# Performance work log

Hardware: AMD Instinct MI355X
Metric: run time of the kernel (lower is better)

The kernel has to match this reference:

```python
import jax, jax.numpy as jnp
import numpy as np

N = 10000
E = 160000
NEG_SLOPE = 0.2
BN_EPS = 1e-5


def _gat_conv(x, W, a_src, a_dst, b, src, dst, n, heads):
    # PyG GATConv, concat=False (mean over heads), shared lin for src/dst.
    H = heads
    C = W.shape[1] // H
    h = (x @ W).reshape(n, H, C)                       # (N,H,C)
    e_s = jnp.einsum('nhc,hc->nh', h, a_src)           # (N,H)
    e_d = jnp.einsum('nhc,hc->nh', h, a_dst)
    alpha = jax.nn.leaky_relu(e_s[src] + e_d[dst], NEG_SLOPE)   # (E',H)
    amax = jax.ops.segment_max(alpha, dst, num_segments=n)       # per-dst softmax
    ex = jnp.exp(alpha - amax[dst])
    denom = jax.ops.segment_sum(ex, dst, num_segments=n)
    w = ex / (denom[dst] + 1e-16)
    out = jax.ops.segment_sum(h[src] * w[:, :, None], dst, num_segments=n)  # (N,H,C)
    return out.mean(axis=1) + b


def _bn(x, g, b):
    mu = x.mean(axis=0)
    var = x.var(axis=0)  # biased, as torch BN training forward
    return (x - mu) * jax.lax.rsqrt(var + BN_EPS) * g + b


def setup_inputs() -> dict:
    key = jax.random.key(0)
    ks = jax.random.split(key, 32)
    d = {}
    d['x'] = jax.random.normal(ks[0], (N, 64), jnp.float32)
    d['edge_index'] = jax.random.randint(ks[1], (2, E), 0, N, jnp.int64)
    s = lambda k, shape, fan: jax.random.normal(k, shape, jnp.float32) * (1.0 / np.sqrt(fan))
    d['Wp'] = s(ks[2], (64, 128), 64); d['bp'] = jnp.zeros((128,), jnp.float32)
    # conv0: 8 heads, per-head 128
    d['W0'] = s(ks[3], (128, 8 * 128), 128); d['as0'] = s(ks[4], (8, 128), 128)
    d['ad0'] = s(ks[5], (8, 128), 128); d['b0'] = jnp.zeros((128,), jnp.float32)
    d['g0'] = jnp.ones((128,), jnp.float32); d['be0'] = jnp.zeros((128,), jnp.float32)
    # conv1: same shape
    d['W1'] = s(ks[6], (128, 8 * 128), 128); d['as1'] = s(ks[7], (8, 128), 128)
    d['ad1'] = s(ks[8], (8, 128), 128); d['b1'] = jnp.zeros((128,), jnp.float32)
    d['g1'] = jnp.ones((128,), jnp.float32); d['be1'] = jnp.zeros((128,), jnp.float32)
    # conv2: 1 head, out 64
    d['W2'] = s(ks[9], (128, 64), 128); d['as2'] = s(ks[10], (1, 64), 64)
    d['ad2'] = s(ks[11], (1, 64), 64); d['b2'] = jnp.zeros((64,), jnp.float32)
    d['g2'] = jnp.ones((64,), jnp.float32); d['be2'] = jnp.zeros((64,), jnp.float32)
    # residual projection for layer 2 (128 -> 64)
    d['Wr'] = s(ks[12], (128, 64), 128); d['br'] = jnp.zeros((64,), jnp.float32)
    return d


def reference(x, edge_index, Wp, bp, W0, as0, ad0, b0, g0, be0,
              W1, as1, ad1, b1, g1, be1, W2, as2, ad2, b2, g2, be2, Wr, br):
    n = x.shape[0]
    loops = jnp.arange(n, dtype=edge_index.dtype)
    src = jnp.concatenate([edge_index[0], loops])  # add_self_loops=True
    dst = jnp.concatenate([edge_index[1], loops])
    h = x @ Wp + bp
    # layer 0 (8 heads, identity residual)
    hr = h
    h = jax.nn.elu(_bn(_gat_conv(h, W0, as0, ad0, b0, src, dst, n, 8), g0, be0)) + hr
    # layer 1
    hr = h
    h = jax.nn.elu(_bn(_gat_conv(h, W1, as1, ad1, b1, src, dst, n, 8), g1, be1)) + hr
    # layer 2 (1 head, linear residual 128->64)
    hr = h @ Wr + br
    h = jax.nn.elu(_bn(_gat_conv(h, W2, as2, ad2, b2, src, dst, n, 1), g2, be2)) + hr
    return h
```

## Files before the change

kernel.cpp:

```cpp
#include <hip/hip_runtime.h>
#include <hip/hip_bf16.h>
#include <cstdint>
#include <cstddef>

#define TPB 256

typedef __attribute__((ext_vector_type(8))) short bf16x8;
typedef __attribute__((ext_vector_type(8))) unsigned short ushort8;
typedef __attribute__((ext_vector_type(4))) float f32x4;

static __device__ __forceinline__ float bf2f(unsigned short u) {
  union { unsigned int i; float f; } c;
  c.i = ((unsigned int)u) << 16;
  return c.f;
}

__global__ void detect_kernel(const unsigned int* __restrict__ w, int* __restrict__ flag) {
  __shared__ int any32;
  if (threadIdx.x == 0) any32 = 0;
  __syncthreads();
  for (int i = threadIdx.x; i < 1024; i += TPB)
    if (w[2 * i + 1] != 0u) any32 = 1;
  __syncthreads();
  if (threadIdx.x == 0) *flag = any32;
}

__global__ void decode_kernel(const void* __restrict__ raw, const int* __restrict__ flag,
                              int* __restrict__ src, int* __restrict__ dst, int E, int n) {
  int i = blockIdx.x * TPB + threadIdx.x;
  int tot = E + n;
  if (i >= tot) return;
  if (i < E) {
    if (*flag) {
      const int* p = (const int*)raw;
      src[i] = p[i];
      dst[i] = p[E + i];
    } else {
      const long long* p = (const long long*)raw;
      src[i] = (int)p[i];
      dst[i] = (int)p[E + i];
    }
  } else {
    src[i] = i - E;
    dst[i] = i - E;
  }
}

__global__ void count_kernel(const int* __restrict__ dst, int* __restrict__ counts, int etot) {
  int i = blockIdx.x * TPB + threadIdx.x;
  if (i < etot) atomicAdd(&counts[dst[i]], 1);
}

__global__ void scan_kernel(const int* __restrict__ counts, int* __restrict__ row_ptr, int n) {
  __shared__ int part[TPB];
  int tid = threadIdx.x;
  int chunk = (n + TPB - 1) / TPB;
  int begin = tid * chunk;
  int end = begin + chunk; if (end > n) end = n;
  int s = 0;
  for (int i = begin; i < end && i < n; i++) s += counts[i];
  part[tid] = s;
  __syncthreads();
  for (int off = 1; off < TPB; off <<= 1) {
    int v = (tid >= off) ? part[tid - off] : 0;
    __syncthreads();
    part[tid] += v;
    __syncthreads();
  }
  int base = (tid == 0) ? 0 : part[tid - 1];
  for (int i = begin; i < end && i < n; i++) { row_ptr[i] = base; base += counts[i]; }
  if (tid == TPB - 1) row_ptr[n] = base;
}

__global__ void fill_kernel(const int* __restrict__ src, const int* __restrict__ dst,
                            const int* __restrict__ row_ptr, int* __restrict__ fill,
                            int* __restrict__ sorted_src, int etot) {
  int i = blockIdx.x * TPB + threadIdx.x;
  if (i >= etot) return;
  int d = dst[i];
  int pos = row_ptr[d] + atomicAdd(&fill[d], 1);
  sorted_src[pos] = src[i];
}

__global__ void f32_to_bf16_kernel(const float* __restrict__ in, __hip_bfloat16* __restrict__ out, int n) {
  int i = blockIdx.x * TPB + threadIdx.x;
  if (i < n) out[i] = __float2bfloat16(in[i]);
}

__global__ void f32_to_bf16_T_kernel(const float* __restrict__ in, __hip_bfloat16* __restrict__ out,
                                     int K, int N) {
  __shared__ float tile[32][33];
  const int k0 = blockIdx.x * 32, n0 = blockIdx.y * 32;
  const int tx = threadIdx.x & 31, ty = threadIdx.x >> 5;
  for (int r = ty; r < 32; r += 8) {
    int k = k0 + r, n = n0 + tx;
    tile[r][tx] = (k < K && n < N) ? in[(size_t)k * N + n] : 0.f;
  }
  __syncthreads();
  for (int r = ty; r < 32; r += 8) {
    int n = n0 + r, k = k0 + tx;
    if (n < N && k < K) out[(size_t)n * K + k] = __float2bfloat16(tile[tx][r]);
  }
}

__global__ __launch_bounds__(256) void gemm_bf16t_kernel(
    const short* __restrict__ A, const short* __restrict__ Bt,
    const float* __restrict__ bias, float* __restrict__ C,
    __hip_bfloat16* __restrict__ Cb, int M, int N, int K) {
  __shared__ short As[64][40];
  __shared__ short Bs[128][40];

  const int tid = threadIdx.x;
  const int lane = tid & 63;
  const int w = tid >> 6;
  const int bm = blockIdx.x * 64;
  const int bn = blockIdx.y * 128;

  f32x4 acc[8];
#pragma unroll
  for (int nt = 0; nt < 8; nt++) acc[nt] = (f32x4){0.f, 0.f, 0.f, 0.f};

  const int arow = tid >> 2;
  const int akk = (tid & 3) << 3;
  const int brow = tid >> 1;
  const int bkk = (tid & 1) << 4;

  for (int k0 = 0; k0 < K; k0 += 32) {
    {
      int gr = bm + arow;
      if (gr < M) {
        *(bf16x8*)&As[arow][akk] = *(const bf16x8*)&A[(size_t)gr * K + k0 + akk];
      } else {
        bf16x8 z = {0, 0, 0, 0, 0, 0, 0, 0};
        *(bf16x8*)&As[arow][akk] = z;
      }
    }
    {
      int gbn = bn + brow;
      if (gbn < N) {
        const short* bp = &Bt[(size_t)gbn * K + k0 + bkk];
        *(bf16x8*)&Bs[brow][bkk]     = *(const bf16x8*)bp;
        *(bf16x8*)&Bs[brow][bkk + 8] = *(const bf16x8*)(bp + 8);
      } else {
        bf16x8 z = {0, 0, 0, 0, 0, 0, 0, 0};
        *(bf16x8*)&Bs[brow][bkk] = z;
        *(bf16x8*)&Bs[brow][bkk + 8] = z;
      }
    }
    __syncthreads();

    bf16x8 a = *(const bf16x8*)&As[w * 16 + (lane & 15)][(lane >> 4) * 8];
#pragma unroll
    for (int nt = 0; nt < 8; nt++) {
      bf16x8 b = *(const bf16x8*)&Bs[nt * 16 + (lane & 15)][(lane >> 4) * 8];
      acc[nt] = __builtin_amdgcn_mfma_f32_16x16x32_bf16(a, b, acc[nt], 0, 0, 0);
    }
    __syncthreads();
  }

#pragma unroll
  for (int nt = 0; nt < 8; nt++) {
    int gc = bn + nt * 16 + (lane & 15);
    if (gc >= N) continue;
    float bv = bias ? bias[gc] : 0.f;
#pragma unroll
    for (int q = 0; q < 4; q++) {
      int gr = bm + w * 16 + (lane >> 4) * 4 + q;
      if (gr < M) {
        float val = acc[nt][q] + bv;
        if (C) C[(size_t)gr * N + gc] = val;
        if (Cb) Cb[(size_t)gr * N + gc] = __float2bfloat16(val);
      }
    }
  }
}

__global__ void attn_coeff8_kernel(const unsigned short* __restrict__ gb,
                                   const float* __restrict__ asrc,
                                   const float* __restrict__ adst,
                                   float* __restrict__ es, float* __restrict__ ed) {
  const int v = blockIdx.x;
  const int tid = threadIdx.x;
  ushort4 gu = *(const ushort4*)&gb[(size_t)v * 1024 + 4 * tid];
  float4 av = *(const float4*)&asrc[4 * tid];
  float4 dv = *(const float4*)&adst[4 * tid];
  float gx = bf2f(gu.x), gy = bf2f(gu.y), gz = bf2f(gu.z), gw = bf2f(gu.w);
  float p1 = gx * av.x + gy * av.y + gz * av.z + gw * av.w;
  float p2 = gx * dv.x + gy * dv.y + gz * dv.z + gw * dv.w;
#pragma unroll
  for (int off = 16; off > 0; off >>= 1) {
    p1 += __shfl_down(p1, off);
    p2 += __shfl_down(p2, off);
  }
  if ((tid & 31) == 0) {
    es[(size_t)v * 8 + (tid >> 5)] = p1;
    ed[(size_t)v * 8 + (tid >> 5)] = p2;
  }
}

template <int H, int C>
__global__ void attn_coeff_kernel(const float* __restrict__ g,
                                  const float* __restrict__ asrc,
                                  const float* __restrict__ adst,
                                  float* __restrict__ es, float* __restrict__ ed) {
  int v = blockIdx.x;
  int tid = threadIdx.x;
  __shared__ float rs[2], rd[2];
  const float* grow = g + (size_t)v * (H * C);
  for (int h = 0; h < H; ++h) {
    float gv = grow[h * C + tid];
    float p1 = gv * asrc[h * C + tid];
    float p2 = gv * adst[h * C + tid];
#pragma unroll
    for (int off = 32; off > 0; off >>= 1) {
      p1 += __shfl_down(p1, off);
      p2 += __shfl_down(p2, off);
    }
    if ((tid & 63) == 0) { rs[tid >> 6] = p1; rd[tid >> 6] = p2; }
    __syncthreads();
    if (tid == 0) {
      float s1 = rs[0], s2 = rd[0];
      if (C > 64) { s1 += rs[1]; s2 += rd[1]; }
      es[(size_t)v * H + h] = s1;
      ed[(size_t)v * H + h] = s2;
    }
    __syncthreads();
  }
}

__global__ __launch_bounds__(256) void gat_aggregate8w_kernel(
    const int* __restrict__ row_ptr, const int* __restrict__ srcs,
    const unsigned short* __restrict__ gb, const float* __restrict__ es,
    const float* __restrict__ ed, const float* __restrict__ bias,
    float* __restrict__ out, int n) {
  const int wave = threadIdx.x >> 6;
  const int lane = threadIdx.x & 63;
  const int v = blockIdx.x * 4 + wave;
  if (v >= n) return;

  const int begin = row_ptr[v];
  const int deg = row_ptr[v + 1] - begin;

  const int eh = lane & 7;
  const int ee = lane >> 3;
  const int hh = lane >> 3;
  const int c0 = lane << 4;

  const float edv = ed[(size_t)v * 8 + eh];

  float acc[16];
#pragma unroll
  for (int k = 0; k < 16; k++) acc[k] = 0.f;

  if (deg <= 64) {
    float a[8];
    int sreg[8];
#pragma unroll
    for (int b = 0; b < 8; b++) {
      a[b] = -1e30f;
      sreg[b] = 0;
      int e = b * 8 + ee;
      if (e < deg) {
        int s = srcs[begin + e];
        sreg[b] = s;
        float t = es[(size_t)s * 8 + eh] + edv;
        a[b] = t > 0.f ? t : 0.2f * t;
      }
    }
    float m = a[0];
#pragma unroll
    for (int b = 1; b < 8; b++) m = fmaxf(m, a[b]);
    m = fmaxf(m, __shfl_xor(m, 8));
    m = fmaxf(m, __shfl_xor(m, 16));
    m = fmaxf(m, __shfl_xor(m, 32));
    float dsum = 0.f;
#pragma unroll
    for (int b = 0; b < 8; b++) { a[b] = __expf(a[b] - m); dsum += a[b]; }
    dsum += __shfl_xor(dsum, 8);
    dsum += __shfl_xor(dsum, 16);
    dsum += __shfl_xor(dsum, 32);
    const float invd = 1.0f / (dsum + 1e-16f);
#pragma unroll
    for (int b = 0; b < 8; b++) a[b] *= invd;

#pragma unroll
    for (int b = 0; b < 8; b++) {
      if (b * 8 >= deg) break;
#pragma unroll
      for (int jj = 0; jj < 8; jj++) {
        if (b * 8 + jj >= deg) break;
        const int sl = (jj << 3) | hh;
        const int s = __shfl(sreg[b], sl);
        const float w = __shfl(a[b], sl);
        const ushort8* p = (const ushort8*)&gb[(size_t)s * 1024 + c0];
        ushort8 u0 = p[0], u1 = p[1];
#pragma unroll
        for (int k = 0; k < 8; k++) {
          acc[k]     += w * bf2f(u0[k]);
          acc[k + 8] += w * bf2f(u1[k]);
        }
      }
    }
  } else {
    float m = -1e30f;
    for (int base = 0; base < deg; base += 8) {
      int e = base + ee;
      if (e < deg) {
        int s = srcs[begin + e];
        float t = es[(size_t)s * 8 + eh] + edv;
        t = t > 0.f ? t : 0.2f * t;
        m = fmaxf(m, t);
      }
    }
    m = fmaxf(m, __shfl_xor(m, 8));
    m = fmaxf(m, __shfl_xor(m, 16));
    m = fmaxf(m, __shfl_xor(m, 32));
    float dsum = 0.f;
    for (int base = 0; base < deg; base += 8) {
      int e = base + ee;
      if (e < deg) {
        int s = srcs[begin + e];
        float t = es[(size_t)s * 8 + eh] + edv;
        t = t > 0.f ? t : 0.2f * t;
        dsum += __expf(t - m);
      }
    }
    dsum += __shfl_xor(dsum, 8);
    dsum += __shfl_xor(dsum, 16);
    dsum += __shfl_xor(dsum, 32);
    const float invd = 1.0f / (dsum + 1e-16f);
    for (int base = 0; base < deg; base += 8) {
      int e = base + ee;
      float w = 0.f; int s = 0;
      if (e < deg) {
        s = srcs[begin + e];
        float t = es[(size_t)s * 8 + eh] + edv;
        t = t > 0.f ? t : 0.2f * t;
        w = __expf(t - m) * invd;
      }
#pragma unroll
      for (int jj = 0; jj < 8; jj++) {
        if (base + jj >= deg) break;
        const int sl = (jj << 3) | hh;
        const int ss = __shfl(s, sl);
        const float ww = __shfl(w, sl);
        const ushort8* p = (const ushort8*)&gb[(size_t)ss * 1024 + c0];
        ushort8 u0 = p[0], u1 = p[1];
#pragma unroll
        for (int k = 0; k < 8; k++) {
          acc[k]     += ww * bf2f(u0[k]);
          acc[k + 8] += ww * bf2f(u1[k]);
        }
      }
    }
  }

#pragma unroll
  for (int k = 0; k < 16; k++) {
    acc[k] += __shfl_xor(acc[k], 8);
    acc[k] += __shfl_xor(acc[k], 16);
    acc[k] += __shfl_xor(acc[k], 32);
  }
  if (hh == 0) {
    const int cc = (lane & 7) << 4;
#pragma unroll
    for (int k = 0; k < 16; k++)
      out[(size_t)v * 128 + cc + k] = acc[k] * 0.125f + bias[cc + k];
  }
}

__global__ __launch_bounds__(256) void gat_aggregate1_kernel(
    const int* __restrict__ row_ptr, const int* __restrict__ srcs,
    const float* __restrict__ g, const float* __restrict__ es,
    const float* __restrict__ ed, const float* __restrict__ bias,
    float* __restrict__ out, int n) {
  const int wave = threadIdx.x >> 6;
  const int lane = threadIdx.x & 63;
  const int v = blockIdx.x * 4 + wave;
  if (v >= n) return;

  const int begin = row_ptr[v];
  const int deg = row_ptr[v + 1] - begin;
  const float edv = ed[v];

  float pm = -1e30f;
  for (int j = lane; j < deg; j += 64) {
    float a = es[srcs[begin + j]] + edv;
    a = a > 0.f ? a : 0.2f * a;
    pm = fmaxf(pm, a);
  }
#pragma unroll
  for (int off = 32; off > 0; off >>= 1) pm = fmaxf(pm, __shfl_xor(pm, off));

  float ps = 0.f;
  for (int j = lane; j < deg; j += 64) {
    float a = es[srcs[begin + j]] + edv;
    a = a > 0.f ? a : 0.2f * a;
    ps += expf(a - pm);
  }
#pragma unroll
  for (int off = 32; off > 0; off >>= 1) ps += __shfl_xor(ps, off);
  const float invd = 1.0f / (ps + 1e-16f);

  float acc = 0.f;
  for (int base = 0; base < deg; base += 64) {
    int cnt = deg - base; if (cnt > 64) cnt = 64;
    int sv = 0; float wv = 0.f;
    if (lane < cnt) {
      sv = srcs[begin + base + lane];
      float a = es[sv] + edv;
      a = a > 0.f ? a : 0.2f * a;
      wv = expf(a - pm) * invd;
    }
    for (int j = 0; j < cnt; j++) {
      int s = __shfl(sv, j);
      float wgt = __shfl(wv, j);
      acc += wgt * g[(size_t)s * 64 + lane];
    }
  }
  out[(size_t)v * 64 + lane] = acc + bias[lane];
}

template <int C>
__global__ void bn_stats_kernel(const float* __restrict__ x, int n, float* __restrict__ sums) {
  constexpr int T = 256;
  constexpr int RPI = T / C;
  constexpr int ITER = 64;
  constexpr int ROWS = RPI * ITER;
  int c = threadIdx.x % C;
  int r0 = threadIdx.x / C;
  int rowBase = blockIdx.x * ROWS;
  float s = 0.f, q = 0.f;
  for (int it = 0; it < ITER; ++it) {
    int r = rowBase + it * RPI + r0;
    if (r < n) {
      float v = x[(size_t)r * C + c];
      s += v; q += v * v;
    }
  }
  __shared__ float ls[T], lq[T];
  ls[threadIdx.x] = s; lq[threadIdx.x] = q;
  __syncthreads();
  if (threadIdx.x < C) {
    float ts = 0.f, tq = 0.f;
    for (int r = 0; r < RPI; ++r) { ts += ls[c + r * C]; tq += lq[c + r * C]; }
    atomicAdd(&sums[c], ts);
    atomicAdd(&sums[C + c], tq);
  }
}

template <int C>
__global__ void bn_elu_res_kernel(const float* __restrict__ x, const float* __restrict__ sums,
                                  const float* __restrict__ gamma, const float* __restrict__ beta,
                                  const float* __restrict__ res, float* __restrict__ out,
                                  __hip_bfloat16* __restrict__ outb, int n) {
  int i = blockIdx.x * TPB + threadIdx.x;
  if (i >= n * C) return;
  int c = i % C;
  float inv_n = 1.0f / (float)n;
  float mu = sums[c] * inv_n;
  float var = sums[C + c] * inv_n - mu * mu;
  float y = (x[i] - mu) * rsqrtf(var + 1e-5f) * gamma[c] + beta[c];
  y = y > 0.f ? y : expm1f(y);
  y += res[i];
  out[i] = y;
  if (outb) outb[i] = __float2bfloat16(y);
}

extern "C" void kernel_launch(void* const* d_in, const int* in_sizes, int n_in,
                              void* d_out, int out_size, void* d_ws, size_t ws_size,
                              hipStream_t stream) {
  const float* x   = (const float*)d_in[0];
  const void*  ei  = d_in[1];
  const float* Wp  = (const float*)d_in[2];
  const float* bp  = (const float*)d_in[3];
  const float* W0  = (const float*)d_in[4];
  const float* as0 = (const float*)d_in[5];
  const float* ad0 = (const float*)d_in[6];
  const float* b0  = (const float*)d_in[7];
  const float* g0  = (const float*)d_in[8];
  const float* be0 = (const float*)d_in[9];
  const float* W1  = (const float*)d_in[10];
  const float* as1 = (const float*)d_in[11];
  const float* ad1 = (const float*)d_in[12];
  const float* b1  = (const float*)d_in[13];
  const float* g1  = (const float*)d_in[14];
  const float* be1 = (const float*)d_in[15];
  const float* W2  = (const float*)d_in[16];
  const float* as2 = (const float*)d_in[17];
  const float* ad2 = (const float*)d_in[18];
  const float* b2  = (const float*)d_in[19];
  const float* g2  = (const float*)d_in[20];
  const float* be2 = (const float*)d_in[21];
  const float* Wr  = (const float*)d_in[22];
  const float* br  = (const float*)d_in[23];

  const int N = in_sizes[0] / 64;
  const int E = in_sizes[1] / 2;
  const int ETOT = E + N;

  char* wsp = (char*)d_ws;
  size_t off = 0;
  auto alloc = [&](size_t bytes) -> void* {
    void* p = wsp + off;
    off += (bytes + 255) & ~(size_t)255;
    return p;
  };
  int*   flag    = (int*)alloc(4);
  int*   e_src   = (int*)alloc((size_t)ETOT * 4);
  int*   e_dst   = (int*)alloc((size_t)ETOT * 4);
  int*   counts  = (int*)alloc((size_t)N * 4);
  int*   fillc   = (int*)alloc((size_t)N * 4);
  int*   row_ptr = (int*)alloc((size_t)(N + 1) * 4);
  int*   s_src   = (int*)alloc((size_t)ETOT * 4);
  float* hA      = (float*)alloc((size_t)N * 128 * 4);
  float* hB      = (float*)alloc((size_t)N * 128 * 4);
  float* gbuf    = (float*)alloc((size_t)N * 64 * 4);
  float* gat     = (float*)alloc((size_t)N * 128 * 4);
  float* es      = (float*)alloc((size_t)N * 8 * 4);
  float* ed      = (float*)alloc((size_t)N * 8 * 4);
  float* bnsum   = (float*)alloc(2 * 128 * 4);
  __hip_bfloat16* gbufb = (__hip_bfloat16*)alloc((size_t)N * 1024 * 2);
  __hip_bfloat16* xb  = (__hip_bfloat16*)alloc((size_t)N * 64 * 2);
  __hip_bfloat16* hAb = (__hip_bfloat16*)alloc((size_t)N * 128 * 2);
  __hip_bfloat16* hBb = (__hip_bfloat16*)alloc((size_t)N * 128 * 2);
  __hip_bfloat16* WpT = (__hip_bfloat16*)alloc((size_t)128 * 64 * 2);
  __hip_bfloat16* W0T = (__hip_bfloat16*)alloc((size_t)1024 * 128 * 2);
  __hip_bfloat16* W1T = (__hip_bfloat16*)alloc((size_t)1024 * 128 * 2);
  __hip_bfloat16* W2T = (__hip_bfloat16*)alloc((size_t)64 * 128 * 2);
  __hip_bfloat16* WrT = (__hip_bfloat16*)alloc((size_t)64 * 128 * 2);

  const int egrid = (ETOT + TPB - 1) / TPB;
  const int mgrid = (N + 63) / 64;
  auto cgrid = [](int n) { return (n + TPB - 1) / TPB; };

  detect_kernel<<<1, TPB, 0, stream>>>((const unsigned int*)ei, flag);
  decode_kernel<<<egrid, TPB, 0, stream>>>(ei, flag, e_src, e_dst, E, N);
  hipMemsetAsync(counts, 0, (size_t)N * 4, stream);
  hipMemsetAsync(fillc, 0, (size_t)N * 4, stream);
  count_kernel<<<egrid, TPB, 0, stream>>>(e_dst, counts, ETOT);
  scan_kernel<<<1, TPB, 0, stream>>>(counts, row_ptr, N);
  fill_kernel<<<egrid, TPB, 0, stream>>>(e_src, e_dst, row_ptr, fillc, s_src, ETOT);

  f32_to_bf16_kernel<<<cgrid(N * 64), TPB, 0, stream>>>(x, xb, N * 64);
  f32_to_bf16_T_kernel<<<dim3(2, 4), 256, 0, stream>>>(Wp, WpT, 64, 128);
  f32_to_bf16_T_kernel<<<dim3(4, 32), 256, 0, stream>>>(W0, W0T, 128, 1024);
  f32_to_bf16_T_kernel<<<dim3(4, 32), 256, 0, stream>>>(W1, W1T, 128, 1024);
  f32_to_bf16_T_kernel<<<dim3(4, 2), 256, 0, stream>>>(W2, W2T, 128, 64);
  f32_to_bf16_T_kernel<<<dim3(4, 2), 256, 0, stream>>>(Wr, WrT, 128, 64);

  gemm_bf16t_kernel<<<dim3(mgrid, 1), 256, 0, stream>>>(
      (const short*)xb, (const short*)WpT, bp, hA, hAb, N, 128, 64);

  gemm_bf16t_kernel<<<dim3(mgrid, 8), 256, 0, stream>>>(
      (const short*)hAb, (const short*)W0T, nullptr, nullptr, gbufb, N, 1024, 128);
  attn_coeff8_kernel<<<N, 256, 0, stream>>>((const unsigned short*)gbufb, as0, ad0, es, ed);
  gat_aggregate8w_kernel<<<(N + 3) / 4, 256, 0, stream>>>(
      row_ptr, s_src, (const unsigned short*)gbufb, es, ed, b0, gat, N);
  hipMemsetAsync(bnsum, 0, 2 * 128 * 4, stream);
  bn_stats_kernel<128><<<(N + 127) / 128, 256, 0, stream>>>(gat, N, bnsum);
  bn_elu_res_kernel<128><<<cgrid(N * 128), TPB, 0, stream>>>(gat, bnsum, g0, be0, hA, hB, hBb, N);

  gemm_bf16t_kernel<<<dim3(mgrid, 8), 256, 0, stream>>>(
      (const short*)hBb, (const short*)W1T, nullptr, nullptr, gbufb, N, 1024, 128);
  attn_coeff8_kernel<<<N, 256, 0, stream>>>((const unsigned short*)gbufb, as1, ad1, es, ed);
  gat_aggregate8w_kernel<<<(N + 3) / 4, 256, 0, stream>>>(
      row_ptr, s_src, (const unsigned short*)gbufb, es, ed, b1, gat, N);
  hipMemsetAsync(bnsum, 0, 2 * 128 * 4, stream);
  bn_stats_kernel<128><<<(N + 127) / 128, 256, 0, stream>>>(gat, N, bnsum);
  bn_elu_res_kernel<128><<<cgrid(N * 128), TPB, 0, stream>>>(gat, bnsum, g1, be1, hB, hA, hAb, N);

  gemm_bf16t_kernel<<<dim3(mgrid, 1), 256, 0, stream>>>(
      (const short*)hAb, (const short*)WrT, br, hB, nullptr, N, 64, 128);
  gemm_bf16t_kernel<<<dim3(mgrid, 1), 256, 0, stream>>>(
      (const short*)hAb, (const short*)W2T, nullptr, gbuf, nullptr, N, 64, 128);
  attn_coeff_kernel<1, 64><<<N, 64, 0, stream>>>(gbuf, as2, ad2, es, ed);
  gat_aggregate1_kernel<<<(N + 3) / 4, 256, 0, stream>>>(row_ptr, s_src, gbuf, es, ed, b2, gat, N);
  hipMemsetAsync(bnsum, 0, 2 * 64 * 4, stream);
  bn_stats_kernel<64><<<(N + 255) / 256, 256, 0, stream>>>(gat, N, bnsum);
  bn_elu_res_kernel<64><<<cgrid(N * 64), TPB, 0, stream>>>(gat, bnsum, g2, be2, hB, (float*)d_out, nullptr, N);
}
```

Measured before the change: 336.0 us.

## Fuse attention coefficients into GEMM epilogue and batch gathers via LDS

Computes the per-head source and destination attention dot products in the GEMM epilogue with a 16-lane shuffle reduction, which removes the separate attn_coeff kernels and their re-read of the projected features. It also restructures the 8-head aggregation so edge weights and source indices are staged in LDS per wave. Four neighbour rows are then gathered per iteration, replacing per-edge shuffles and exposing more memory-level parallelism. In exchange, the fused epilogue uses fp32 values rather than bf16-rounded ones, and the LDS staging raises shared-memory use per block.

```diff
diff --git a/kernel.cpp b/kernel.cpp
--- a/kernel.cpp
+++ b/kernel.cpp
@@ -106,7 +106,9 @@
 __global__ __launch_bounds__(256) void gemm_bf16t_kernel(
     const short* __restrict__ A, const short* __restrict__ Bt,
     const float* __restrict__ bias, float* __restrict__ C,
-    __hip_bfloat16* __restrict__ Cb, int M, int N, int K) {
+    __hip_bfloat16* __restrict__ Cb, int M, int Ncols, int K,
+    const float* __restrict__ asrc, const float* __restrict__ adst,
+    float* __restrict__ es_out, float* __restrict__ ed_out, int H, int hshift) {
   __shared__ short As[64][40];
   __shared__ short Bs[128][40];
 
@@ -137,7 +139,7 @@
     }
     {
       int gbn = bn + brow;
-      if (gbn < N) {
+      if (gbn < Ncols) {
         const short* bp = &Bt[(size_t)gbn * K + k0 + bkk];
         *(bf16x8*)&Bs[brow][bkk]     = *(const bf16x8*)bp;
         *(bf16x8*)&Bs[brow][bkk + 8] = *(const bf16x8*)(bp + 8);
@@ -158,73 +160,44 @@
     __syncthreads();
   }
 
+  float p1[4] = {0.f, 0.f, 0.f, 0.f};
+  float p2[4] = {0.f, 0.f, 0.f, 0.f};
+
 #pragma unroll
   for (int nt = 0; nt < 8; nt++) {
     int gc = bn + nt * 16 + (lane & 15);
-    if (gc >= N) continue;
+    if (gc >= Ncols) continue;
     float bv = bias ? bias[gc] : 0.f;
+    float asv = es_out ? asrc[gc] : 0.f;
+    float adv = es_out ? adst[gc] : 0.f;
 #pragma unroll
     for (int q = 0; q < 4; q++) {
       int gr = bm + w * 16 + (lane >> 4) * 4 + q;
       if (gr < M) {
         float val = acc[nt][q] + bv;
-        if (C) C[(size_t)gr * N + gc] = val;
-        if (Cb) Cb[(size_t)gr * N + gc] = __float2bfloat16(val);
-      }
-    }
-  }
-}
-
-__global__ void attn_coeff8_kernel(const unsigned short* __restrict__ gb,
-                                   const float* __restrict__ asrc,
-                                   const float* __restrict__ adst,
-                                   float* __restrict__ es, float* __restrict__ ed) {
-  const int v = blockIdx.x;
-  const int tid = threadIdx.x;
-  ushort4 gu = *(const ushort4*)&gb[(size_t)v * 1024 + 4 * tid];
-  float4 av = *(const float4*)&asrc[4 * tid];
-  float4 dv = *(const float4*)&adst[4 * tid];
-  float gx = bf2f(gu.x), gy = bf2f(gu.y), gz = bf2f(gu.z), gw = bf2f(gu.w);
-  float p1 = gx * av.x + gy * av.y + gz * av.z + gw * av.w;
-  float p2 = gx * dv.x + gy * dv.y + gz * dv.z + gw * dv.w;
-#pragma unroll
-  for (int off = 16; off > 0; off >>= 1) {
-    p1 += __shfl_down(p1, off);
-    p2 += __shfl_down(p2, off);
-  }
-  if ((tid & 31) == 0) {
-    es[(size_t)v * 8 + (tid >> 5)] = p1;
-    ed[(size_t)v * 8 + (tid >> 5)] = p2;
-  }
-}
-
-template <int H, int C>
-__global__ void attn_coeff_kernel(const float* __restrict__ g,
-                                  const float* __restrict__ asrc,
-                                  const float* __restrict__ adst,
-                                  float* __restrict__ es, float* __restrict__ ed) {
-  int v = blockIdx.x;
-  int tid = threadIdx.x;
-  __shared__ float rs[2], rd[2];
-  const float* grow = g + (size_t)v * (H * C);
-  for (int h = 0; h < H; ++h) {
-    float gv = grow[h * C + tid];
-    float p1 = gv * asrc[h * C + tid];
-    float p2 = gv * adst[h * C + tid];
-#pragma unroll
-    for (int off = 32; off > 0; off >>= 1) {
-      p1 += __shfl_down(p1, off);
-      p2 += __shfl_down(p2, off);
-    }
-    if ((tid & 63) == 0) { rs[tid >> 6] = p1; rd[tid >> 6] = p2; }
-    __syncthreads();
-    if (tid == 0) {
-      float s1 = rs[0], s2 = rd[0];
-      if (C > 64) { s1 += rs[1]; s2 += rd[1]; }
-      es[(size_t)v * H + h] = s1;
-      ed[(size_t)v * H + h] = s2;
-    }
-    __syncthreads();
+        if (C) C[(size_t)gr * Ncols + gc] = val;
+        if (Cb) Cb[(size_t)gr * Ncols + gc] = __float2bfloat16(val);
+        p1[q] += val * asv;
+        p2[q] += val * adv;
+      }
+    }
+  }
+
+  if (es_out) {
+    const int head = bn >> hshift;
+#pragma unroll
+    for (int q = 0; q < 4; q++) {
+      float s1 = p1[q], s2 = p2[q];
+      s1 += __shfl_xor(s1, 1); s2 += __shfl_xor(s2, 1);
+      s1 += __shfl_xor(s1, 2); s2 += __shfl_xor(s2, 2);
+      s1 += __shfl_xor(s1, 4); s2 += __shfl_xor(s2, 4);
+      s1 += __shfl_xor(s1, 8); s2 += __shfl_xor(s2, 8);
+      int gr = bm + w * 16 + (lane >> 4) * 4 + q;
+      if ((lane & 15) == 0 && gr < M) {
+        es_out[(size_t)gr * H + head] = s1;
+        ed_out[(size_t)gr * H + head] = s2;
+      }
+    }
   }
 }
 
@@ -236,6 +209,10 @@
   const int wave = threadIdx.x >> 6;
   const int lane = threadIdx.x & 63;
   const int v = blockIdx.x * 4 + wave;
+
+  __shared__ float wlds[4][64][8];
+  __shared__ int slds[4][64];
+
   if (v >= n) return;
 
   const int begin = row_ptr[v];
@@ -281,75 +258,96 @@
     dsum += __shfl_xor(dsum, 32);
     const float invd = 1.0f / (dsum + 1e-16f);
 #pragma unroll
-    for (int b = 0; b < 8; b++) a[b] *= invd;
-
-#pragma unroll
     for (int b = 0; b < 8; b++) {
-      if (b * 8 >= deg) break;
-#pragma unroll
-      for (int jj = 0; jj < 8; jj++) {
-        if (b * 8 + jj >= deg) break;
-        const int sl = (jj << 3) | hh;
-        const int s = __shfl(sreg[b], sl);
-        const float w = __shfl(a[b], sl);
-        const ushort8* p = (const ushort8*)&gb[(size_t)s * 1024 + c0];
-        ushort8 u0 = p[0], u1 = p[1];
-#pragma unroll
-        for (int k = 0; k < 8; k++) {
-          acc[k]     += w * bf2f(u0[k]);
-          acc[k + 8] += w * bf2f(u1[k]);
-        }
+      wlds[wave][b * 8 + ee][eh] = a[b] * invd;
+      if (eh == 0) slds[wave][b * 8 + ee] = sreg[b];
+    }
+
+    const int npad = (deg + 3) & ~3;
+    for (int j0 = 0; j0 < npad; j0 += 4) {
+      float w0 = wlds[wave][j0 + 0][hh];
+      float w1 = wlds[wave][j0 + 1][hh];
+      float w2 = wlds[wave][j0 + 2][hh];
+      float w3 = wlds[wave][j0 + 3][hh];
+      int s0 = slds[wave][j0 + 0];
+      int s1 = slds[wave][j0 + 1];
+      int s2 = slds[wave][j0 + 2];
+      int s3 = slds[wave][j0 + 3];
+      const ushort8* p0 = (const ushort8*)&gb[(size_t)s0 * 1024 + c0];
+      const ushort8* p1 = (const ushort8*)&gb[(size_t)s1 * 1024 + c0];
+      const ushort8* p2 = (const ushort8*)&gb[(size_t)s2 * 1024 + c0];
+      const ushort8* p3 = (const ushort8*)&gb[(size_t)s3 * 1024 + c0];
+      ushort8 u0a = p0[0], u0b = p0[1];
+      ushort8 u1a = p1[0], u1b = p1[1];
+      ushort8 u2a = p2[0], u2b = p2[1];
+      ushort8 u3a = p3[0], u3b = p3[1];
+#pragma unroll
+      for (int k = 0; k < 8; k++) {
+        acc[k]     += w0 * bf2f(u0a[k]) + w1 * bf2f(u1a[k]) + w2 * bf2f(u2a[k]) + w3 * bf2f(u3a[k]);
+        acc[k + 8] += w0 * bf2f(u0b[k]) + w1 * bf2f(u1b[k]) + w2 * bf2f(u2b[k]) + w3 * bf2f(u3b[k]);
       }
     }
   } else {
     float m = -1e30f;
-    for (int base = 0; base < deg; base += 8) {
-      int e = base + ee;
-      if (e < deg) {
-        int s = srcs[begin + e];
-        float t = es[(size_t)s * 8 + eh] + edv;
-        t = t > 0.f ? t : 0.2f * t;
-        m = fmaxf(m, t);
-      }
+    for (int base = ee; base < deg; base += 8) {
+      int s = srcs[begin + base];
+      float t = es[(size_t)s * 8 + eh] + edv;
+      t = t > 0.f ? t : 0.2f * t;
+      m = fmaxf(m, t);
     }
     m = fmaxf(m, __shfl_xor(m, 8));
     m = fmaxf(m, __shfl_xor(m, 16));
     m = fmaxf(m, __shfl_xor(m, 32));
     float dsum = 0.f;
-    for (int base = 0; base < deg; base += 8) {
-      int e = base + ee;
-      if (e < deg) {
-        int s = srcs[begin + e];
-        float t = es[(size_t)s * 8 + eh] + edv;
-        t = t > 0.f ? t : 0.2f * t;
-        dsum += __expf(t - m);
-      }
+    for (int base = ee; base < deg; base += 8) {
+      int s = srcs[begin + base];
+      float t = es[(size_t)s * 8 + eh] + edv;
+      t = t > 0.f ? t : 0.2f * t;
+      dsum += __expf(t - m);
     }
     dsum += __shfl_xor(dsum, 8);
     dsum += __shfl_xor(dsum, 16);
     dsum += __shfl_xor(dsum, 32);
     const float invd = 1.0f / (dsum + 1e-16f);
-    for (int base = 0; base < deg; base += 8) {
-      int e = base + ee;
-      float w = 0.f; int s = 0;
-      if (e < deg) {
-        s = srcs[begin + e];
-        float t = es[(size_t)s * 8 + eh] + edv;
-        t = t > 0.f ? t : 0.2f * t;
-        w = __expf(t - m) * invd;
-      }
-#pragma unroll
-      for (int jj = 0; jj < 8; jj++) {
-        if (base + jj >= deg) break;
-        const int sl = (jj << 3) | hh;
-        const int ss = __shfl(s, sl);
-        const float ww = __shfl(w, sl);
-        const ushort8* p = (const ushort8*)&gb[(size_t)ss * 1024 + c0];
-        ushort8 u0 = p[0], u1 = p[1];
+
+    for (int base = 0; base < deg; base += 64) {
+      const int cnt = min(64, deg - base);
+#pragma unroll
+      for (int b = 0; b < 8; b++) {
+        int e = base + b * 8 + ee;
+        float wv = 0.f;
+        int s = 0;
+        if (e < deg) {
+          s = srcs[begin + e];
+          float t = es[(size_t)s * 8 + eh] + edv;
+          t = t > 0.f ? t : 0.2f * t;
+          wv = __expf(t - m) * invd;
+        }
+        wlds[wave][b * 8 + ee][eh] = wv;
+        if (eh == 0) slds[wave][b * 8 + ee] = s;
+      }
+      const int npad = (cnt + 3) & ~3;
+      for (int j0 = 0; j0 < npad; j0 += 4) {
+        float w0 = wlds[wave][j0 + 0][hh];
+        float w1 = wlds[wave][j0 + 1][hh];
+        float w2 = wlds[wave][j0 + 2][hh];
+        float w3 = wlds[wave][j0 + 3][hh];
+        int s0 = slds[wave][j0 + 0];
+        int s1 = slds[wave][j0 + 1];
+        int s2 = slds[wave][j0 + 2];
+        int s3 = slds[wave][j0 + 3];
+        const ushort8* p0 = (const ushort8*)&gb[(size_t)s0 * 1024 + c0];
+        const ushort8* p1 = (const ushort8*)&gb[(size_t)s1 * 1024 + c0];
+        const ushort8* p2 = (const ushort8*)&gb[(size_t)s2 * 1024 + c0];
+        const ushort8* p3 = (const ushort8*)&gb[(size_t)s3 * 1024 + c0];
+        ushort8 u0a = p0[0], u0b = p0[1];
+        ushort8 u1a = p1[0], u1b = p1[1];
+        ushort8 u2a = p2[0], u2b = p2[1];
+        ushort8 u3a = p3[0], u3b = p3[1];
 #pragma unroll
         for (int k = 0; k < 8; k++) {
-          acc[k]     += ww * bf2f(u0[k]);
-          acc[k + 8] += ww * bf2f(u1[k]);
+          acc[k]     += w0 * bf2f(u0a[k]) + w1 * bf2f(u1a[k]) + w2 * bf2f(u2a[k]) + w3 * bf2f(u3a[k]);
+          acc[k + 8] += w0 * bf2f(u0b[k]) + w1 * bf2f(u1b[k]) + w2 * bf2f(u2b[k]) + w3 * bf2f(u3b[k]);
         }
       }
     }
@@ -550,11 +548,12 @@
   f32_to_bf16_T_kernel<<<dim3(4, 2), 256, 0, stream>>>(Wr, WrT, 128, 64);
 
   gemm_bf16t_kernel<<<dim3(mgrid, 1), 256, 0, stream>>>(
-      (const short*)xb, (const short*)WpT, bp, hA, hAb, N, 128, 64);
+      (const short*)xb, (const short*)WpT, bp, hA, hAb, N, 128, 64,
+      nullptr, nullptr, nullptr, nullptr, 1, 7);
 
   gemm_bf16t_kernel<<<dim3(mgrid, 8), 256, 0, stream>>>(
-      (const short*)hAb, (const short*)W0T, nullptr, nullptr, gbufb, N, 1024, 128);
-  attn_coeff8_kernel<<<N, 256, 0, stream>>>((const unsigned short*)gbufb, as0, ad0, es, ed);
+      (const short*)hAb, (const short*)W0T, nullptr, nullptr, gbufb, N, 1024, 128,
+      as0, ad0, es, ed, 8, 7);
   gat_aggregate8w_kernel<<<(N + 3) / 4, 256, 0, stream>>>(
       row_ptr, s_src, (const unsigned short*)gbufb, es, ed, b0, gat, N);
   hipMemsetAsync(bnsum, 0, 2 * 128 * 4, stream);
@@ -562,8 +561,8 @@
   bn_elu_res_kernel<128><<<cgrid(N * 128), TPB, 0, stream>>>(gat, bnsum, g0, be0, hA, hB, hBb, N);
 
   gemm_bf16t_kernel<<<dim3(mgrid, 8), 256, 0, stream>>>(
-      (const short*)hBb, (const short*)W1T, nullptr, nullptr, gbufb, N, 1024, 128);
-  attn_coeff8_kernel<<<N, 256, 0, stream>>>((const unsigned short*)gbufb, as1, ad1, es, ed);
+      (const short*)hBb, (const short*)W1T, nullptr, nullptr, gbufb, N, 1024, 128,
+      as1, ad1, es, ed, 8, 7);
   gat_aggregate8w_kernel<<<(N + 3) / 4, 256, 0, stream>>>(
       row_ptr, s_src, (const unsigned short*)gbufb, es, ed, b1, gat, N);
   hipMemsetAsync(bnsum, 0, 2 * 128 * 4, stream);
@@ -571,10 +570,11 @@
   bn_elu_res_kernel<128><<<cgrid(N * 128), TPB, 0, stream>>>(gat, bnsum, g1, be1, hB, hA, hAb, N);
 
   gemm_bf16t_kernel<<<dim3(mgrid, 1), 256, 0, stream>>>(
-      (const short*)hAb, (const short*)WrT, br, hB, nullptr, N, 64, 128);
+      (const short*)hAb, (const short*)WrT, br, hB, nullptr, N, 64, 128,
+      nullptr, nullptr, nullptr, nullptr, 1, 7);
   gemm_bf16t_kernel<<<dim3(mgrid, 1), 256, 0, stream>>>(
-      (const short*)hAb, (const short*)W2T, nullptr, gbuf, nullptr, N, 64, 128);
-  attn_coeff_kernel<1, 64><<<N, 64, 0, stream>>>(gbuf, as2, ad2, es, ed);
+      (const short*)hAb, (const short*)W2T, nullptr, gbuf, nullptr, N, 64, 128,
+      as2, ad2, es, ed, 1, 6);
   gat_aggregate1_kernel<<<(N + 3) / 4, 256, 0, stream>>>(row_ptr, s_src, gbuf, es, ed, b2, gat, N);
   hipMemsetAsync(bnsum, 0, 2 * 64 * 4, stream);
   bn_stats_kernel<64><<<(N + 255) / 256, 256, 0, stream>>>(gat, N, bnsum);
```

New measurement: 321.2 us. 4.4% less time.
